# Kernel optimization log

Measured on AMD Instinct MI355X. Metric: run time of the kernel, lower is better.

The kernel has to match this reference:

```python
import jax, jax.numpy as jnp
import numpy as np

EPS = 0.1
MAX_ITER = 100
THRESH = 0.1


def _M(C, u, v):
    # (-C + u_i + v_j) / eps, shape [B, N, M]
    return (-C + u[..., :, None] + v[..., None, :]) / EPS


def setup_inputs() -> dict:
    key = jax.random.key(0)
    kx, ky = jax.random.split(key)
    x = jax.random.normal(kx, (8, 2048, 32), dtype=jnp.float32)
    y = jax.random.normal(ky, (8, 2048, 32), dtype=jnp.float32)
    return {"x": x, "y": y}


def reference(x, y):
    # cost matrix: sum |x_i - y_j|^2 over features -> [B, N, M]
    C = jnp.sum(jnp.abs(x[..., :, None, :] - y[..., None, :, :]) ** 2, axis=-1)
    B, N = x.shape[0], x.shape[-2]
    Mp = y.shape[-2]
    log_mu = jnp.log(jnp.full((B, N), 1.0 / N, dtype=C.dtype) + 1e-8)
    log_nu = jnp.log(jnp.full((B, Mp), 1.0 / Mp, dtype=C.dtype) + 1e-8)

    def step(carry, _):
        u, v, done = carry
        u_new = EPS * (log_mu - jax.scipy.special.logsumexp(_M(C, u, v), axis=-1)) + u
        v_new = EPS * (log_nu - jax.scipy.special.logsumexp(_M(C, u_new, v), axis=-2)) + v
        err = jnp.mean(jnp.sum(jnp.abs(u_new - u), axis=-1))
        # honor the original early-break: once err < thresh, freeze u, v
        u = jnp.where(done, u, u_new)
        v = jnp.where(done, v, v_new)
        done = done | (err < THRESH)
        return (u, v, done), None

    u0 = jnp.zeros((B, N), dtype=C.dtype)
    v0 = jnp.zeros((B, Mp), dtype=C.dtype)
    (u, v, _), _ = jax.lax.scan(step, (u0, v0, jnp.array(False)), None, length=MAX_ITER)

    pi = jnp.exp(_M(C, u, v))
    cost = jnp.sum(pi * C, axis=(-2, -1))  # reduction='none' -> [B]
    return cost, pi, C
```

## Files before the change

kernel.cpp:

```cpp
#include <hip/hip_runtime.h>
#include <math.h>

#define EPSF     0.1f
#define BB       8
#define NN       2048
#define DIM      32
#define MAX_ITER 100
#define THRESHF  0.1f
#define SAFE_ITERS 6
#define C20L2E 28.853900817779268f
#define C10L2E 14.426950408889634f
#define LN2F   0.6931471805599453f
#define M2INV  -0.06931471805599453f

typedef __attribute__((ext_vector_type(8))) short  sh8;
typedef __attribute__((ext_vector_type(4))) float  f32x4;

__device__ __forceinline__ float ex2(float x) { return __builtin_amdgcn_exp2f(x); }
__device__ __forceinline__ float lg2(float x) { return __builtin_amdgcn_logf(x); }

__device__ __forceinline__ float coh_load(const float* p) {
  return __uint_as_float(__hip_atomic_load((const unsigned*)p, __ATOMIC_RELAXED,
                                           __HIP_MEMORY_SCOPE_AGENT));
}
__device__ __forceinline__ void coh_store(float* p, float v) {
  __hip_atomic_store((unsigned*)p, __float_as_uint(v), __ATOMIC_RELAXED,
                     __HIP_MEMORY_SCOPE_AGENT);
}

__device__ __forceinline__ unsigned short bf16_rne(float v) {
  unsigned u = __float_as_uint(v);
  unsigned r = (u + 0x7FFFu + ((u >> 16) & 1u)) >> 16;
  return (unsigned short)r;
}

__global__ __launch_bounds__(256) void prep_kernel(const float* __restrict__ in,
                                                   unsigned short* __restrict__ hi,
                                                   unsigned short* __restrict__ lo,
                                                   float* __restrict__ snorm,
                                                   float* __restrict__ w2init,
                                                   float scale) {
  const int tid = blockIdx.x * 256 + threadIdx.x;
  const int row = tid >> 5, k = tid & 31;
  float val = in[tid];
  float vs = val * scale;
  unsigned short h = bf16_rne(vs);
  float hf = __uint_as_float(((unsigned)h) << 16);
  unsigned short l = bf16_rne(vs - hf);
  hi[tid] = h;
  lo[tid] = l;
  float sq = val * val;
#pragma unroll
  for (int off = 1; off < 32; off <<= 1) sq += __shfl_xor(sq, off, 64);
  if (k == 0) {
    snorm[row] = sq;
    w2init[row] = -sq * C10L2E;
  }
  (void)k;
}

__device__ __forceinline__ void batch_barrier(int* __restrict__ cnt, int target) {
  __syncthreads();
  if (threadIdx.x == 0) {
    asm volatile("s_waitcnt vmcnt(0)" ::: "memory");
    __hip_atomic_fetch_add(cnt, 1, __ATOMIC_RELAXED, __HIP_MEMORY_SCOPE_AGENT);
    while (__hip_atomic_load(cnt, __ATOMIC_RELAXED, __HIP_MEMORY_SCOPE_AGENT) < target) {
      __builtin_amdgcn_s_sleep(1);
    }
  }
  __syncthreads();
}

template <bool REC, bool FAST>
__device__ __forceinline__ void sweep_phase(
    const sh8 a0h, const sh8 a0l, const sh8 a1h, const sh8 a1l,
    const unsigned short* __restrict__ Bh, const unsigned short* __restrict__ Bl,
    float* __restrict__ wself2, const float* __restrict__ woth2,
    float* __restrict__ errSlot,
    const int b, const int i0, const float cst, const float sav, float& uold,
    float lm[32][8], float ls[32][8], float* __restrict__ wlds,
    float* __restrict__ mbArr) {
  const int w    = threadIdx.x >> 6;
  const int lane = threadIdx.x & 63;
  const int l15  = lane & 15, q = lane >> 4;
  const int jbase = w * 256;

#pragma unroll
  for (int idx = 0; idx < NN / 512; idx++)
    wlds[idx * 512 + threadIdx.x] = coh_load(&woth2[b * NN + idx * 512 + threadIdx.x]);

  float mbias[8];
  if (FAST) {
#pragma unroll
    for (int r = 0; r < 8; r++)
      mbias[r] = mbArr[(r < 4) ? (q * 4 + r) : (16 + q * 4 + (r & 3))];
  }

  float m2[8], ss[8];
#pragma unroll
  for (int r = 0; r < 8; r++) { m2[r] = -1e30f; ss[r] = 0.f; }

  __syncthreads();

#pragma unroll 2
  for (int tj = 0; tj < 16; tj++) {
    const int j = jbase + tj * 16;
    const size_t brow = ((size_t)(b * NN + j + l15)) * DIM + q * 8;
    const sh8 bh = *(const sh8*)(Bh + brow);
    const sh8 bl = *(const sh8*)(Bl + brow);
    const float wj = wlds[j + l15];
    f32x4 acc0, acc1;
    if (FAST) {
      acc0[0] = wj - mbias[0]; acc0[1] = wj - mbias[1];
      acc0[2] = wj - mbias[2]; acc0[3] = wj - mbias[3];
      acc1[0] = wj - mbias[4]; acc1[1] = wj - mbias[5];
      acc1[2] = wj - mbias[6]; acc1[3] = wj - mbias[7];
    } else {
      acc0[0] = wj; acc0[1] = wj; acc0[2] = wj; acc0[3] = wj;
      acc1 = acc0;
    }
    acc0 = __builtin_amdgcn_mfma_f32_16x16x32_bf16(a0h, bh, acc0, 0, 0, 0);
    acc1 = __builtin_amdgcn_mfma_f32_16x16x32_bf16(a1h, bh, acc1, 0, 0, 0);
    acc0 = __builtin_amdgcn_mfma_f32_16x16x32_bf16(a0h, bl, acc0, 0, 0, 0);
    acc1 = __builtin_amdgcn_mfma_f32_16x16x32_bf16(a1h, bl, acc1, 0, 0, 0);
    acc0 = __builtin_amdgcn_mfma_f32_16x16x32_bf16(a0l, bh, acc0, 0, 0, 0);
    acc1 = __builtin_amdgcn_mfma_f32_16x16x32_bf16(a1l, bh, acc1, 0, 0, 0);
#pragma unroll
    for (int r = 0; r < 8; r++) {
      const float t = (r < 4) ? acc0[r & 3] : acc1[r & 3];
      if (FAST) {
        ss[r] += ex2(t);
      } else {
        const float d = t - m2[r];
        const float e = ex2(-fabsf(d));
        const bool up = d > 0.f;
        ss[r] = up ? fmaf(ss[r], e, 1.f) : (ss[r] + e);
        m2[r] = fmaxf(m2[r], t);
      }
    }
  }

#pragma unroll
  for (int off = 1; off < 16; off <<= 1) {
#pragma unroll
    for (int r = 0; r < 8; r++) {
      if (FAST) {
        ss[r] += __shfl_xor(ss[r], off, 64);
      } else {
        const float mo = __shfl_xor(m2[r], off, 64);
        const float so = __shfl_xor(ss[r], off, 64);
        const float mn = fmaxf(m2[r], mo);
        ss[r] = ss[r] * ex2(m2[r] - mn) + so * ex2(mo - mn);
        m2[r] = mn;
      }
    }
  }

  if (l15 == 0) {
#pragma unroll
    for (int r = 0; r < 4; r++) {
      ls[q * 4 + r][w] = ss[r];
      ls[16 + q * 4 + r][w] = ss[4 + r];
      if (!FAST) {
        lm[q * 4 + r][w] = m2[r];
        lm[16 + q * 4 + r][w] = m2[4 + r];
      }
    }
  }
  __syncthreads();
  if (threadIdx.x < 32) {
    const int row = threadIdx.x;
    float lse2;
    if (FAST) {
      float s = 0.f;
#pragma unroll
      for (int p = 0; p < 8; p++) s += ls[row][p];
      lse2 = mbArr[row] + lg2(s);
    } else {
      float m = lm[row][0], s = ls[row][0];
#pragma unroll
      for (int p = 1; p < 8; p++) {
        const float mo = lm[row][p], so = ls[row][p];
        const float mn = fmaxf(m, mo);
        s = s * ex2(m - mn) + so * ex2(mo - mn);
        m = mn;
      }
      lse2 = m + lg2(s);
    }
    mbArr[row] = lse2;
    const float lse = lse2 * LN2F;
    const int gi = b * NN + i0 + row;
    const float nu = cst + sav - EPSF * lse;
    coh_store(&wself2[gi], (nu - sav) * C10L2E);
    if (REC) {
      float du = fabsf(nu - uold);
#pragma unroll
      for (int off = 1; off < 32; off <<= 1) du += __shfl_xor(du, off, 64);
      if (threadIdx.x == 0) atomicAdd(errSlot, du);
      uold = nu;
    }
  }
  __syncthreads();
}

template <bool PASS1>
__global__ __launch_bounds__(512, 4) void solve_kernel(
    const unsigned short* __restrict__ xh, const unsigned short* __restrict__ xl,
    const unsigned short* __restrict__ yh, const unsigned short* __restrict__ yl,
    const float* __restrict__ sx, const float* __restrict__ sy,
    float* __restrict__ wu2, float* __restrict__ wv2,
    float* __restrict__ errTab, int* __restrict__ gcnt,
    const int* __restrict__ nIterDev,
    float emu, float enu) {
  __shared__ float lm[32][8];
  __shared__ float ls[32][8];
  __shared__ float wlds[NN];
  __shared__ float mbu[32];
  __shared__ float mbv[32];
  const int b  = blockIdx.x & 7;
  const int i0 = (blockIdx.x >> 3) * 32;
  const int nIter = PASS1 ? MAX_ITER : *nIterDev;
  if (nIter == 0) return;

  const int lane = threadIdx.x & 63;
  const int l15 = lane & 15, q = lane >> 4;

  const size_t arow0 = ((size_t)(b * NN + i0 + l15)) * DIM + q * 8;
  const sh8 xa0h = *(const sh8*)(xh + arow0);
  const sh8 xa0l = *(const sh8*)(xl + arow0);
  const sh8 xa1h = *(const sh8*)(xh + arow0 + 16 * DIM);
  const sh8 xa1l = *(const sh8*)(xl + arow0 + 16 * DIM);
  const sh8 ya0h = *(const sh8*)(yh + arow0);
  const sh8 ya0l = *(const sh8*)(yl + arow0);
  const sh8 ya1h = *(const sh8*)(yh + arow0 + 16 * DIM);
  const sh8 ya1l = *(const sh8*)(yl + arow0 + 16 * DIM);

  float savx = 0.f, savy = 0.f, uold = 0.f, dummy = 0.f;
  if (threadIdx.x < 32) {
    savx = sx[b * NN + i0 + threadIdx.x];
    savy = sy[b * NN + i0 + threadIdx.x];
  }

  int* cnt = &gcnt[b * 32];
  int tgt = (PASS1 ? 0 : 2 * MAX_ITER) * 64;

  for (int it = 0; it < nIter; ++it) {
    if (it < SAFE_ITERS)
      sweep_phase<PASS1, false>(xa0h, xa0l, xa1h, xa1l, yh, yl, wu2, wv2,
                                PASS1 ? &errTab[it * BB + b] : wu2,
                                b, i0, emu, savx, uold, lm, ls, wlds, mbu);
    else
      sweep_phase<PASS1, true>(xa0h, xa0l, xa1h, xa1l, yh, yl, wu2, wv2,
                               PASS1 ? &errTab[it * BB + b] : wu2,
                               b, i0, emu, savx, uold, lm, ls, wlds, mbu);
    tgt += 64;
    batch_barrier(cnt, tgt);
    if (it < SAFE_ITERS)
      sweep_phase<false, false>(ya0h, ya0l, ya1h, ya1l, xh, xl, wv2, wu2, wu2,
                                b, i0, enu, savy, dummy, lm, ls, wlds, mbv);
    else
      sweep_phase<false, true>(ya0h, ya0l, ya1h, ya1l, xh, xl, wv2, wu2, wu2,
                               b, i0, enu, savy, dummy, lm, ls, wlds, mbv);
    tgt += 64;
    batch_barrier(cnt, tgt);
  }
}

__global__ __launch_bounds__(256) void tstar_kernel(const float* __restrict__ errTab,
                                                    int* __restrict__ nIterDev,
                                                    const float* __restrict__ sx,
                                                    const float* __restrict__ sy,
                                                    float* __restrict__ wu2,
                                                    float* __restrict__ wv2) {
  __shared__ int best;
  if (threadIdx.x == 0) best = MAX_ITER;
  __syncthreads();
  if (threadIdx.x < MAX_ITER) {
    float e = 0.f;
#pragma unroll
    for (int bb = 0; bb < BB; bb++) e += errTab[threadIdx.x * BB + bb];
    if (e * 0.125f < THRESHF) atomicMin(&best, (int)threadIdx.x);
  }
  __syncthreads();
  const int T = best;
  const int n2 = (T < MAX_ITER - 1) ? T + 1 : 0;
  if (threadIdx.x == 0) *nIterDev = n2;
  if (n2 > 0) {
    for (int idx = threadIdx.x; idx < BB * NN; idx += 256) {
      wu2[idx] = -sx[idx] * C10L2E;
      wv2[idx] = -sy[idx] * C10L2E;
    }
  }
}

__global__ __launch_bounds__(256) void finalize_kernel(const unsigned short* __restrict__ xh,
                                                       const unsigned short* __restrict__ xl,
                                                       const unsigned short* __restrict__ yh,
                                                       const unsigned short* __restrict__ yl,
                                                       const float* __restrict__ sx,
                                                       const float* __restrict__ sy,
                                                       const float* __restrict__ wu2,
                                                       const float* __restrict__ wv2,
                                                       float* __restrict__ C,
                                                       float* __restrict__ pi,
                                                       float* __restrict__ cost) {
  const int b  = blockIdx.z;
  const int wv = threadIdx.x >> 6;
  const int lane = threadIdx.x & 63;
  const int l15 = lane & 15, q = lane >> 4;
  const int i0 = blockIdx.y * 128 + wv * 32;
  const int j0 = blockIdx.x * 256;

  const size_t arow0 = ((size_t)(b * NN + i0 + l15)) * DIM + q * 8;
  const sh8 a0h = *(const sh8*)(xh + arow0);
  const sh8 a0l = *(const sh8*)(xl + arow0);
  const sh8 a1h = *(const sh8*)(xh + arow0 + 16 * DIM);
  const sh8 a1l = *(const sh8*)(xl + arow0 + 16 * DIM);

  float sx0[8], wu0[8];
#pragma unroll
  for (int r = 0; r < 8; r++) {
    const int gi = b * NN + i0 + ((r < 4) ? (q * 4 + (r & 3)) : (16 + q * 4 + (r & 3)));
    sx0[r] = sx[gi];
    wu0[r] = wu2[gi];
  }

  float acc = 0.f;
#pragma unroll 2
  for (int tj = 0; tj < 16; tj++) {
    const int j = j0 + tj * 16;
    const size_t brow = ((size_t)(b * NN + j + l15)) * DIM + q * 8;
    const sh8 bh = *(const sh8*)(yh + brow);
    const sh8 bl = *(const sh8*)(yl + brow);
    f32x4 acc0 = {0.f, 0.f, 0.f, 0.f};
    f32x4 acc1 = {0.f, 0.f, 0.f, 0.f};
    acc0 = __builtin_amdgcn_mfma_f32_16x16x32_bf16(a0h, bh, acc0, 0, 0, 0);
    acc1 = __builtin_amdgcn_mfma_f32_16x16x32_bf16(a1h, bh, acc1, 0, 0, 0);
    acc0 = __builtin_amdgcn_mfma_f32_16x16x32_bf16(a0h, bl, acc0, 0, 0, 0);
    acc1 = __builtin_amdgcn_mfma_f32_16x16x32_bf16(a1h, bl, acc1, 0, 0, 0);
    acc0 = __builtin_amdgcn_mfma_f32_16x16x32_bf16(a0l, bh, acc0, 0, 0, 0);
    acc1 = __builtin_amdgcn_mfma_f32_16x16x32_bf16(a1l, bh, acc1, 0, 0, 0);
    const int gj = b * NN + j + l15;
    const float syj = sy[gj];
    const float wvj = wv2[gj];
#pragma unroll
    for (int r = 0; r < 8; r++) {
      const float Sp = (r < 4) ? acc0[r & 3] : acc1[r & 3];
      const int irow = i0 + ((r < 4) ? (q * 4 + (r & 3)) : (16 + q * 4 + (r & 3)));
      const float Cv = fmaf(M2INV, Sp, sx0[r] + syj);
      const float p  = ex2(Sp + (wu0[r] + wvj));
      const size_t addr = ((size_t)(b * NN + irow)) * NN + j + l15;
      C[addr]  = Cv;
      pi[addr] = p;
      acc = fmaf(p, Cv, acc);
    }
  }
#pragma unroll
  for (int off = 1; off < 64; off <<= 1) acc += __shfl_xor(acc, off, 64);
  __shared__ float red[4];
  if (lane == 0) red[wv] = acc;
  __syncthreads();
  if (threadIdx.x == 0) atomicAdd(&cost[b], red[0] + red[1] + red[2] + red[3]);
}

extern "C" void kernel_launch(void* const* d_in, const int* in_sizes, int n_in,
                              void* d_out, int out_size, void* d_ws, size_t ws_size,
                              hipStream_t stream) {
  const float* x = (const float*)d_in[0];
  const float* y = (const float*)d_in[1];
  float* out  = (float*)d_out;
  float* cost = out;
  float* pi   = out + 8;
  float* C    = out + 8 + (size_t)BB * NN * NN;

  float* ws = (float*)d_ws;
  const int BN = BB * NN;
  float* wu2 = ws;
  float* wv2 = ws + BN;
  float* sx  = ws + 2 * BN;
  float* sy  = ws + 3 * BN;
  float* errTab = ws + 4 * BN;
  int*   gcnt   = (int*)(ws + 4 * BN + 1024);
  int*   nIterDev = (int*)(ws + 4 * BN + 1280);
  unsigned short* xh = (unsigned short*)(ws + 4 * BN + 1536);
  const size_t NE = (size_t)BB * NN * DIM;
  unsigned short* xl = xh + NE;
  unsigned short* yh = xh + 2 * NE;
  unsigned short* yl = xh + 3 * NE;

  hipMemsetAsync(errTab, 0, 1536 * sizeof(float), stream);
  hipMemsetAsync(d_out, 0, 8 * sizeof(float), stream);

  prep_kernel<<<2048, 256, 0, stream>>>(x, xh, xl, sx, wu2, C20L2E);
  prep_kernel<<<2048, 256, 0, stream>>>(y, yh, yl, sy, wv2, 1.0f);

  const float emu = (float)(0.1 * log(1.0 / 2048.0 + 1e-8));
  const float enu = emu;

  solve_kernel<true><<<512, 512, 0, stream>>>(xh, xl, yh, yl, sx, sy, wu2, wv2,
                                              errTab, gcnt, nIterDev, emu, enu);
  tstar_kernel<<<1, 256, 0, stream>>>(errTab, nIterDev, sx, sy, wu2, wv2);
  solve_kernel<false><<<512, 512, 0, stream>>>(xh, xl, yh, yl, sx, sy, wu2, wv2,
                                               errTab, gcnt, nIterDev, emu, enu);

  finalize_kernel<<<dim3(8, 16, BB), 256, 0, stream>>>(xh, xl, yh, yl, sx, sy,
                                                       wu2, wv2, C, pi, cost);
}
```

Measured before the change: 3.295 ms.

## Double rows per block to 64, halving grid and per-batch barrier participants

Each solve block now handles 64 rows instead of 32, so every B-tile load and LDS weight read is reused across four MFMA row groups instead of two. The grid shrinks from 512 to 256 persistent blocks, and each batch barrier waits for 32 arrivals instead of 64. A-operand fragments are now reloaded from global memory in every sweep phase rather than held in registers for the whole solve, and the LDS copy of the weights uses 64-bit loads. In exchange, register pressure per thread rises (launch bounds drop to 2 blocks per CU) and fewer blocks are left to hide latency.

```diff
diff --git a/kernel.cpp b/kernel.cpp
--- a/kernel.cpp
+++ b/kernel.cpp
@@ -8,6 +8,7 @@
 #define MAX_ITER 100
 #define THRESHF  0.1f
 #define SAFE_ITERS 6
+#define BPB      32
 #define C20L2E 28.853900817779268f
 #define C10L2E 14.426950408889634f
 #define LN2F   0.6931471805599453f
@@ -73,32 +74,46 @@
 
 template <bool REC, bool FAST>
 __device__ __forceinline__ void sweep_phase(
-    const sh8 a0h, const sh8 a0l, const sh8 a1h, const sh8 a1l,
+    const unsigned short* __restrict__ Ah, const unsigned short* __restrict__ Al,
     const unsigned short* __restrict__ Bh, const unsigned short* __restrict__ Bl,
     float* __restrict__ wself2, const float* __restrict__ woth2,
     float* __restrict__ errSlot,
     const int b, const int i0, const float cst, const float sav, float& uold,
-    float lm[32][8], float ls[32][8], float* __restrict__ wlds,
+    float lm[64][8], float ls[64][8], float* __restrict__ wlds,
     float* __restrict__ mbArr) {
   const int w    = threadIdx.x >> 6;
   const int lane = threadIdx.x & 63;
   const int l15  = lane & 15, q = lane >> 4;
   const int jbase = w * 256;
 
-#pragma unroll
-  for (int idx = 0; idx < NN / 512; idx++)
-    wlds[idx * 512 + threadIdx.x] = coh_load(&woth2[b * NN + idx * 512 + threadIdx.x]);
-
-  float mbias[8];
+  {
+    const unsigned long long* src = (const unsigned long long*)(woth2 + b * NN);
+    unsigned long long* dst = (unsigned long long*)wlds;
+#pragma unroll
+    for (int idx = 0; idx < 2; idx++)
+      dst[idx * 512 + threadIdx.x] =
+          __hip_atomic_load(src + idx * 512 + threadIdx.x, __ATOMIC_RELAXED,
+                            __HIP_MEMORY_SCOPE_AGENT);
+  }
+
+  const size_t abase = ((size_t)(b * NN + i0 + l15)) * DIM + q * 8;
+  sh8 ah[4], al[4];
+#pragma unroll
+  for (int g = 0; g < 4; g++) {
+    ah[g] = *(const sh8*)(Ah + abase + (size_t)g * 16 * DIM);
+    al[g] = *(const sh8*)(Al + abase + (size_t)g * 16 * DIM);
+  }
+
+  float mbias[16];
   if (FAST) {
 #pragma unroll
-    for (int r = 0; r < 8; r++)
-      mbias[r] = mbArr[(r < 4) ? (q * 4 + r) : (16 + q * 4 + (r & 3))];
-  }
-
-  float m2[8], ss[8];
-#pragma unroll
-  for (int r = 0; r < 8; r++) { m2[r] = -1e30f; ss[r] = 0.f; }
+    for (int r = 0; r < 16; r++)
+      mbias[r] = mbArr[(r >> 2) * 16 + q * 4 + (r & 3)];
+  }
+
+  float m2[16], ss[16];
+#pragma unroll
+  for (int r = 0; r < 16; r++) { m2[r] = -1e30f; ss[r] = 0.f; }
 
   __syncthreads();
 
@@ -109,25 +124,30 @@
     const sh8 bh = *(const sh8*)(Bh + brow);
     const sh8 bl = *(const sh8*)(Bl + brow);
     const float wj = wlds[j + l15];
-    f32x4 acc0, acc1;
-    if (FAST) {
-      acc0[0] = wj - mbias[0]; acc0[1] = wj - mbias[1];
-      acc0[2] = wj - mbias[2]; acc0[3] = wj - mbias[3];
-      acc1[0] = wj - mbias[4]; acc1[1] = wj - mbias[5];
-      acc1[2] = wj - mbias[6]; acc1[3] = wj - mbias[7];
-    } else {
-      acc0[0] = wj; acc0[1] = wj; acc0[2] = wj; acc0[3] = wj;
-      acc1 = acc0;
-    }
-    acc0 = __builtin_amdgcn_mfma_f32_16x16x32_bf16(a0h, bh, acc0, 0, 0, 0);
-    acc1 = __builtin_amdgcn_mfma_f32_16x16x32_bf16(a1h, bh, acc1, 0, 0, 0);
-    acc0 = __builtin_amdgcn_mfma_f32_16x16x32_bf16(a0h, bl, acc0, 0, 0, 0);
-    acc1 = __builtin_amdgcn_mfma_f32_16x16x32_bf16(a1h, bl, acc1, 0, 0, 0);
-    acc0 = __builtin_amdgcn_mfma_f32_16x16x32_bf16(a0l, bh, acc0, 0, 0, 0);
-    acc1 = __builtin_amdgcn_mfma_f32_16x16x32_bf16(a1l, bh, acc1, 0, 0, 0);
-#pragma unroll
-    for (int r = 0; r < 8; r++) {
-      const float t = (r < 4) ? acc0[r & 3] : acc1[r & 3];
+    f32x4 acc[4];
+#pragma unroll
+    for (int g = 0; g < 4; g++) {
+      if (FAST) {
+        acc[g][0] = wj - mbias[g * 4 + 0];
+        acc[g][1] = wj - mbias[g * 4 + 1];
+        acc[g][2] = wj - mbias[g * 4 + 2];
+        acc[g][3] = wj - mbias[g * 4 + 3];
+      } else {
+        acc[g][0] = wj; acc[g][1] = wj; acc[g][2] = wj; acc[g][3] = wj;
+      }
+    }
+#pragma unroll
+    for (int g = 0; g < 4; g++)
+      acc[g] = __builtin_amdgcn_mfma_f32_16x16x32_bf16(ah[g], bh, acc[g], 0, 0, 0);
+#pragma unroll
+    for (int g = 0; g < 4; g++)
+      acc[g] = __builtin_amdgcn_mfma_f32_16x16x32_bf16(ah[g], bl, acc[g], 0, 0, 0);
+#pragma unroll
+    for (int g = 0; g < 4; g++)
+      acc[g] = __builtin_amdgcn_mfma_f32_16x16x32_bf16(al[g], bh, acc[g], 0, 0, 0);
+#pragma unroll
+    for (int r = 0; r < 16; r++) {
+      const float t = acc[r >> 2][r & 3];
       if (FAST) {
         ss[r] += ex2(t);
       } else {
@@ -143,7 +163,7 @@
 #pragma unroll
   for (int off = 1; off < 16; off <<= 1) {
 #pragma unroll
-    for (int r = 0; r < 8; r++) {
+    for (int r = 0; r < 16; r++) {
       if (FAST) {
         ss[r] += __shfl_xor(ss[r], off, 64);
       } else {
@@ -158,17 +178,14 @@
 
   if (l15 == 0) {
 #pragma unroll
-    for (int r = 0; r < 4; r++) {
-      ls[q * 4 + r][w] = ss[r];
-      ls[16 + q * 4 + r][w] = ss[4 + r];
-      if (!FAST) {
-        lm[q * 4 + r][w] = m2[r];
-        lm[16 + q * 4 + r][w] = m2[4 + r];
-      }
-    }
-  }
-  __syncthreads();
-  if (threadIdx.x < 32) {
+    for (int r = 0; r < 16; r++) {
+      const int row = (r >> 2) * 16 + q * 4 + (r & 3);
+      ls[row][w] = ss[r];
+      if (!FAST) lm[row][w] = m2[r];
+    }
+  }
+  __syncthreads();
+  if (threadIdx.x < 64) {
     const int row = threadIdx.x;
     float lse2;
     if (FAST) {
@@ -195,7 +212,7 @@
     if (REC) {
       float du = fabsf(nu - uold);
 #pragma unroll
-      for (int off = 1; off < 32; off <<= 1) du += __shfl_xor(du, off, 64);
+      for (int off = 1; off < 64; off <<= 1) du += __shfl_xor(du, off, 64);
       if (threadIdx.x == 0) atomicAdd(errSlot, du);
       uold = nu;
     }
@@ -204,7 +221,7 @@
 }
 
 template <bool PASS1>
-__global__ __launch_bounds__(512, 4) void solve_kernel(
+__global__ __launch_bounds__(512, 2) void solve_kernel(
     const unsigned short* __restrict__ xh, const unsigned short* __restrict__ xl,
     const unsigned short* __restrict__ yh, const unsigned short* __restrict__ yl,
     const float* __restrict__ sx, const float* __restrict__ sy,
@@ -212,56 +229,43 @@
     float* __restrict__ errTab, int* __restrict__ gcnt,
     const int* __restrict__ nIterDev,
     float emu, float enu) {
-  __shared__ float lm[32][8];
-  __shared__ float ls[32][8];
+  __shared__ float lm[64][8];
+  __shared__ float ls[64][8];
   __shared__ float wlds[NN];
-  __shared__ float mbu[32];
-  __shared__ float mbv[32];
+  __shared__ float mbu[64];
+  __shared__ float mbv[64];
   const int b  = blockIdx.x & 7;
-  const int i0 = (blockIdx.x >> 3) * 32;
+  const int i0 = (blockIdx.x >> 3) * 64;
   const int nIter = PASS1 ? MAX_ITER : *nIterDev;
   if (nIter == 0) return;
 
-  const int lane = threadIdx.x & 63;
-  const int l15 = lane & 15, q = lane >> 4;
-
-  const size_t arow0 = ((size_t)(b * NN + i0 + l15)) * DIM + q * 8;
-  const sh8 xa0h = *(const sh8*)(xh + arow0);
-  const sh8 xa0l = *(const sh8*)(xl + arow0);
-  const sh8 xa1h = *(const sh8*)(xh + arow0 + 16 * DIM);
-  const sh8 xa1l = *(const sh8*)(xl + arow0 + 16 * DIM);
-  const sh8 ya0h = *(const sh8*)(yh + arow0);
-  const sh8 ya0l = *(const sh8*)(yl + arow0);
-  const sh8 ya1h = *(const sh8*)(yh + arow0 + 16 * DIM);
-  const sh8 ya1l = *(const sh8*)(yl + arow0 + 16 * DIM);
-
   float savx = 0.f, savy = 0.f, uold = 0.f, dummy = 0.f;
-  if (threadIdx.x < 32) {
+  if (threadIdx.x < 64) {
     savx = sx[b * NN + i0 + threadIdx.x];
     savy = sy[b * NN + i0 + threadIdx.x];
   }
 
   int* cnt = &gcnt[b * 32];
-  int tgt = (PASS1 ? 0 : 2 * MAX_ITER) * 64;
+  int tgt = (PASS1 ? 0 : 2 * MAX_ITER) * BPB;
 
   for (int it = 0; it < nIter; ++it) {
     if (it < SAFE_ITERS)
-      sweep_phase<PASS1, false>(xa0h, xa0l, xa1h, xa1l, yh, yl, wu2, wv2,
+      sweep_phase<PASS1, false>(xh, xl, yh, yl, wu2, wv2,
                                 PASS1 ? &errTab[it * BB + b] : wu2,
                                 b, i0, emu, savx, uold, lm, ls, wlds, mbu);
     else
-      sweep_phase<PASS1, true>(xa0h, xa0l, xa1h, xa1l, yh, yl, wu2, wv2,
+      sweep_phase<PASS1, true>(xh, xl, yh, yl, wu2, wv2,
                                PASS1 ? &errTab[it * BB + b] : wu2,
                                b, i0, emu, savx, uold, lm, ls, wlds, mbu);
-    tgt += 64;
+    tgt += BPB;
     batch_barrier(cnt, tgt);
     if (it < SAFE_ITERS)
-      sweep_phase<false, false>(ya0h, ya0l, ya1h, ya1l, xh, xl, wv2, wu2, wu2,
+      sweep_phase<false, false>(yh, yl, xh, xl, wv2, wu2, wu2,
                                 b, i0, enu, savy, dummy, lm, ls, wlds, mbv);
     else
-      sweep_phase<false, true>(ya0h, ya0l, ya1h, ya1l, xh, xl, wv2, wu2, wu2,
+      sweep_phase<false, true>(yh, yl, xh, xl, wv2, wu2, wu2,
                                b, i0, enu, savy, dummy, lm, ls, wlds, mbv);
-    tgt += 64;
+    tgt += BPB;
     batch_barrier(cnt, tgt);
   }
 }
@@ -397,10 +401,10 @@
   const float emu = (float)(0.1 * log(1.0 / 2048.0 + 1e-8));
   const float enu = emu;
 
-  solve_kernel<true><<<512, 512, 0, stream>>>(xh, xl, yh, yl, sx, sy, wu2, wv2,
+  solve_kernel<true><<<256, 512, 0, stream>>>(xh, xl, yh, yl, sx, sy, wu2, wv2,
                                               errTab, gcnt, nIterDev, emu, enu);
   tstar_kernel<<<1, 256, 0, stream>>>(errTab, nIterDev, sx, sy, wu2, wv2);
-  solve_kernel<false><<<512, 512, 0, stream>>>(xh, xl, yh, yl, sx, sy, wu2, wv2,
+  solve_kernel<false><<<256, 512, 0, stream>>>(xh, xl, yh, yl, sx, sy, wu2, wv2,
                                                errTab, gcnt, nIterDev, emu, enu);
 
   finalize_kernel<<<dim3(8, 16, BB), 256, 0, stream>>>(xh, xl, yh, yl, sx, sy,
```

Result: faster. 2.726 ms (-17.3%).
